# Kernel optimization log

Hardware: AMD Instinct MI355X
Metric: run time of the kernel (lower is better)

## Reference

```python
import jax, jax.numpy as jnp
import numpy as np

N, L, H, V = 8192, 512, 64, 50000
NUM_PARENT = 1024


def setup_inputs() -> dict:
    key = jax.random.key(0)
    ks = jax.random.split(key, 12)
    def mat(k, shape):
        return 0.1 * jax.random.normal(k, shape, dtype=jnp.float32)
    return {
        "x_word": jax.random.normal(ks[0], (N, L), dtype=jnp.float32),
        "x_index": jax.random.randint(ks[1], (N, L), 0, V),
        "tree": jax.random.randint(ks[2], (N, 2), 0, N),
        "num_parent": NUM_PARENT,
        "embedding": mat(ks[3], (V, H)),
        "W_z": mat(ks[4], (H, H)),
        "U_z": mat(ks[5], (H, H)),
        "b_z": jnp.zeros((H,), dtype=jnp.float32),
        "W_r": mat(ks[6], (H, H)),
        "U_r": mat(ks[7], (H, H)),
        "b_r": jnp.zeros((H,), dtype=jnp.float32),
        "W_h": mat(ks[8], (H, H)),
        "U_h": mat(ks[9], (H, H)),
        "b_h": jnp.zeros((H,), dtype=jnp.float32),
    }


def _hard_sigmoid(x):
    # torch double-threshold trick == clip(0.2*x + 0.5, 0, 1)
    return jnp.clip(0.2 * x + 0.5, 0.0, 1.0)


def reference(x_word, x_index, tree, num_parent, embedding,
              W_z, U_z, b_z, W_r, U_r, b_r, W_h, U_h, b_h):
    n_nodes = x_word.shape[0]
    hdim = embedding.shape[1]

    def step(node_h, xs):
        word, idx, info = xs  # word: [L] f32, idx: [L] int, info: [2] int
        parent_h = node_h[info[0]]                 # [H]
        child_xe = embedding[idx].T @ word         # [H] weighted embedding sum
        z = _hard_sigmoid(W_z @ child_xe + U_z @ parent_h + b_z)
        r = _hard_sigmoid(W_r @ child_xe + U_r @ parent_h + b_r)
        c = jnp.tanh(W_h @ child_xe + U_h @ (parent_h * r) + b_h)
        h = z * parent_h + (1.0 - z) * c           # [H]
        return node_h.at[info[1]].set(h), h

    node_h0 = jnp.zeros((n_nodes, hdim), dtype=x_word.dtype)
    # original loops i in range(len(x_word) - 1)
    _, child_hs = jax.lax.scan(step, node_h0,
                               (x_word[:-1], x_index[:-1], tree[:-1]))
    # output = max over child_hs[num_parent-1:]
    return jnp.max(child_hs[num_parent - 1:], axis=0)
```

## Files before the change

kernel.cpp:

```cpp
#include <hip/hip_runtime.h>
#include <math.h>

#define NODES  8192
#define STEPS  8191
#define LW     512
#define H      64
#define VOCAB  50000
#define SWEEPK 13

__global__ void ws_too_small_kernel(float* __restrict__ out) {
    if (threadIdx.x < H) out[threadIdx.x] = -12345.0f;
}

__global__ __launch_bounds__(256)
void cvt_emb(const float* __restrict__ emb, unsigned int* __restrict__ embh) {
    int i = blockIdx.x * 256 + threadIdx.x;
    float2 v = reinterpret_cast<const float2*>(emb)[i];
    unsigned int ux = __float_as_uint(v.x);
    unsigned int uy = __float_as_uint(v.y);
    unsigned int bx = (ux + 0x7fffu + ((ux >> 16) & 1u)) >> 16;
    unsigned int by = (uy + 0x7fffu + ((uy >> 16) & 1u)) >> 16;
    embh[i] = bx | (by << 16);
}

__global__ __launch_bounds__(256)
void zero_kernel(int* __restrict__ p) {
    p[blockIdx.x * blockDim.x + threadIdx.x] = 0;
}

__global__ __launch_bounds__(256)
void hist_writers(const int* __restrict__ tree, int* __restrict__ count) {
    int j = blockIdx.x * blockDim.x + threadIdx.x;
    if (j < STEPS) atomicAdd(&count[tree[2 * j + 1]], 1);
}

__global__ __launch_bounds__(1024)
void prefix_kernel(const int* __restrict__ cnt, int* __restrict__ off) {
    __shared__ int wsum[16];
    int tid  = threadIdx.x;
    int lane = tid & 63;
    int wv   = tid >> 6;
    int base = tid * 8;

    int v[8], run = 0;
    #pragma unroll
    for (int e = 0; e < 8; ++e) { v[e] = run; run += cnt[base + e]; }

    int x = run;
    #pragma unroll
    for (int d = 1; d < 64; d <<= 1) {
        int y = __shfl_up(x, d, 64);
        if (lane >= d) x += y;
    }
    if (lane == 63) wsum[wv] = x;
    __syncthreads();
    if (wv == 0) {
        int s = (lane < 16) ? wsum[lane] : 0;
        #pragma unroll
        for (int d = 1; d < 16; d <<= 1) {
            int y = __shfl_up(s, d, 64);
            if (lane >= d) s += y;
        }
        if (lane < 16) wsum[lane] = s;
    }
    __syncthreads();
    int wbase = (wv > 0) ? wsum[wv - 1] : 0;
    int tbase = wbase + x - run;
    #pragma unroll
    for (int e = 0; e < 8; ++e) off[base + e] = tbase + v[e];
    if (tid == 1023) off[8192] = tbase + run;
}

__global__ __launch_bounds__(256)
void scatter_writers(const int* __restrict__ tree, const int* __restrict__ woff,
                     int* __restrict__ cursor, int* __restrict__ writers) {
    int j = blockIdx.x * blockDim.x + threadIdx.x;
    if (j >= STEPS) return;
    int v = tree[2 * j + 1];
    int pos = atomicAdd(&cursor[v], 1);
    writers[woff[v] + pos] = j;
}

__global__ __launch_bounds__(256)
void pred_bucket(const int* __restrict__ tree, const int* __restrict__ woff,
                 const int* __restrict__ writers, int* __restrict__ pred) {
    int i = blockIdx.x * blockDim.x + threadIdx.x;
    if (i >= STEPS) return;
    int v  = tree[2 * i];
    int t0 = woff[v], t1 = woff[v + 1];
    int best = -1;
    for (int t = t0; t < t1; ++t) {
        int j = writers[t];
        if (j < i && j > best) best = j;
    }
    pred[i] = best;
}

__global__ __launch_bounds__(1024)
void fused_sched(const int* __restrict__ pred, int* __restrict__ lstart_g,
                 int* __restrict__ order_g) {
    __shared__ int   smem_i[NODES];
    __shared__ short dep[NODES];
    __shared__ int   wsum[16];
    int tid = threadIdx.x;

    short* jmp = (short*)smem_i;
    for (int i = tid; i < NODES; i += 1024) {
        int p = (i < STEPS) ? pred[i] : -1;
        jmp[i] = (short)p;
        dep[i] = (p >= 0) ? 1 : 0;
    }
    __syncthreads();

    for (int r = 0; r < 13; ++r) {
        short nd[8], nj[8];
        #pragma unroll
        for (int e = 0; e < 8; ++e) {
            int i = tid + e * 1024;
            int j = jmp[i];
            if (j >= 0) { nd[e] = (short)(dep[i] + dep[j]); nj[e] = jmp[j]; }
            else        { nd[e] = dep[i];                   nj[e] = -1;     }
        }
        __syncthreads();
        #pragma unroll
        for (int e = 0; e < 8; ++e) {
            int i = tid + e * 1024;
            dep[i] = nd[e];
            jmp[i] = nj[e];
        }
        __syncthreads();
    }

    int d8[8];
    #pragma unroll
    for (int e = 0; e < 8; ++e) d8[e] = dep[tid + e * 1024];
    __syncthreads();

    int* lcnt = smem_i;
    for (int i = tid; i < NODES; i += 1024) lcnt[i] = 0;
    __syncthreads();
    #pragma unroll
    for (int e = 0; e < 8; ++e) {
        int i = tid + e * 1024;
        if (i < STEPS) atomicAdd(&lcnt[d8[e]], 1);
    }
    __syncthreads();

    {
        int lane = tid & 63, wv = tid >> 6, base = tid * 8;
        int v[8], run = 0;
        #pragma unroll
        for (int e = 0; e < 8; ++e) { v[e] = run; run += lcnt[base + e]; }
        int x = run;
        #pragma unroll
        for (int d = 1; d < 64; d <<= 1) {
            int y = __shfl_up(x, d, 64);
            if (lane >= d) x += y;
        }
        if (lane == 63) wsum[wv] = x;
        __syncthreads();
        if (wv == 0) {
            int s = (lane < 16) ? wsum[lane] : 0;
            #pragma unroll
            for (int d = 1; d < 16; d <<= 1) {
                int y = __shfl_up(s, d, 64);
                if (lane >= d) s += y;
            }
            if (lane < 16) wsum[lane] = s;
        }
        __syncthreads();
        int wbase = (wv > 0) ? wsum[wv - 1] : 0;
        int tbase = wbase + x - run;
        #pragma unroll
        for (int e = 0; e < 8; ++e) lstart_g[base + e] = tbase + v[e];
        if (tid == 1023) lstart_g[8192] = tbase + run;
    }
    __threadfence_block();
    __syncthreads();

    for (int i = tid; i < NODES; i += 1024) lcnt[i] = 0;
    __syncthreads();
    #pragma unroll
    for (int e = 0; e < 8; ++e) {
        int i = tid + e * 1024;
        if (i < STEPS) {
            int d = d8[e];
            int pos = atomicAdd(&lcnt[d], 1);
            order_g[lstart_g[d] + pos] = i;
        }
    }
}

__global__ __launch_bounds__(256)
void gather_project(const float* __restrict__ xw, const int* __restrict__ xi,
                    const unsigned short* __restrict__ embh,
                    const float* __restrict__ Wz, const float* __restrict__ Wr,
                    const float* __restrict__ Wh,
                    const float* __restrict__ bz, const float* __restrict__ br,
                    const float* __restrict__ bh,
                    const int* __restrict__ pred,
                    float* __restrict__ A, float* __restrict__ child_h) {
    int i    = blockIdx.x;
    int tid  = threadIdx.x;
    int wave = tid >> 6;
    int lane = tid & 63;
    int g8   = lane >> 3;
    int h8   = (lane & 7) * 8;

    __shared__ float part[4][64];
    __shared__ float xe[64];

    const float* xwi = xw + (size_t)i * LW;
    const int*   xii = xi + (size_t)i * LW;

    float acc[8] = {0.f, 0.f, 0.f, 0.f, 0.f, 0.f, 0.f, 0.f};
    #pragma unroll 4
    for (int it = 0; it < 16; ++it) {
        int l   = wave * 128 + it * 8 + g8;
        int idx = xii[l];
        float w = xwi[l];
        uint4 q = *reinterpret_cast<const uint4*>(embh + ((size_t)idx << 6) + h8);
        acc[0] = fmaf(w, __uint_as_float(q.x << 16),          acc[0]);
        acc[1] = fmaf(w, __uint_as_float(q.x & 0xffff0000u),  acc[1]);
        acc[2] = fmaf(w, __uint_as_float(q.y << 16),          acc[2]);
        acc[3] = fmaf(w, __uint_as_float(q.y & 0xffff0000u),  acc[3]);
        acc[4] = fmaf(w, __uint_as_float(q.z << 16),          acc[4]);
        acc[5] = fmaf(w, __uint_as_float(q.z & 0xffff0000u),  acc[5]);
        acc[6] = fmaf(w, __uint_as_float(q.w << 16),          acc[6]);
        acc[7] = fmaf(w, __uint_as_float(q.w & 0xffff0000u),  acc[7]);
    }
    #pragma unroll
    for (int c = 0; c < 8; ++c) {
        acc[c] += __shfl_xor(acc[c], 8,  64);
        acc[c] += __shfl_xor(acc[c], 16, 64);
        acc[c] += __shfl_xor(acc[c], 32, 64);
    }
    if (lane < 8) {
        #pragma unroll
        for (int c = 0; c < 8; ++c) part[wave][lane * 8 + c] = acc[c];
    }
    __syncthreads();
    if (tid < 64) xe[tid] = part[0][tid] + part[1][tid] + part[2][tid] + part[3][tid];
    __syncthreads();

    float s = 0.f;
    if (tid < 192) {
        int o = tid & 63;
        const float* W = (tid < 64) ? Wz : (tid < 128 ? Wr : Wh);
        const float* b = (tid < 64) ? bz : (tid < 128 ? br : bh);
        s = b[o];
        #pragma unroll
        for (int j = 0; j < H; j += 4) {
            float4 w4 = *reinterpret_cast<const float4*>(W + (size_t)o * H + j);
            s = fmaf(w4.x, xe[j],     s);
            s = fmaf(w4.y, xe[j + 1], s);
            s = fmaf(w4.z, xe[j + 2], s);
            s = fmaf(w4.w, xe[j + 3], s);
        }
    }
    bool isroot = (pred[i] < 0);
    if (tid < 64)                part[0][tid]       = s;
    if (tid >= 128 && tid < 192) part[1][tid - 128] = s;
    __syncthreads();
    if (isroot) {
        if (tid < 64) {
            float z = fminf(fmaxf(0.2f * part[0][tid] + 0.5f, 0.f), 1.f);
            float c = tanhf(part[1][tid]);
            child_h[(size_t)i * H + tid] = (1.f - z) * c;
        }
    } else {
        if (tid < 192) A[(size_t)i * 192 + tid] = s;
    }
}

__device__ __forceinline__ void gru_core(
        int i, int lane, const float* __restrict__ A,
        const int* __restrict__ pred,
        const float* uz, const float* ur, const float* uh,
        float* __restrict__ child_h) {
    int p = pred[i];
    float ph = (p >= 0) ? child_h[(size_t)p * H + lane] : 0.f;
    const float* Ai = A + (size_t)i * 192;
    float az = Ai[lane];
    float ar = Ai[64 + lane];
    float ah = Ai[128 + lane];

    #pragma unroll
    for (int j = 0; j < H; ++j) {
        float s = __shfl(ph, j, 64);
        az = fmaf(uz[j], s, az);
        ar = fmaf(ur[j], s, ar);
    }
    float z = fminf(fmaxf(0.2f * az + 0.5f, 0.f), 1.f);
    float r = fminf(fmaxf(0.2f * ar + 0.5f, 0.f), 1.f);
    float phr = ph * r;
    #pragma unroll
    for (int j = 0; j < H; ++j) {
        float s = __shfl(phr, j, 64);
        ah = fmaf(uh[j], s, ah);
    }
    float c = tanhf(ah);
    child_h[(size_t)i * H + lane] = z * ph + (1.f - z) * c;
}

__global__ __launch_bounds__(256)
void sweep_lvl(int k, const int* __restrict__ lstart, const int* __restrict__ order,
               const float* __restrict__ A, const int* __restrict__ pred,
               const float* __restrict__ Uz, const float* __restrict__ Ur,
               const float* __restrict__ Uh, float* __restrict__ child_h) {
    int s0 = lstart[k], s1 = lstart[k + 1];
    int wave = (blockIdx.x * blockDim.x + threadIdx.x) >> 6;
    int lane = threadIdx.x & 63;
    if (s0 + wave >= s1) return;

    float uz[H], ur[H], uh[H];
    #pragma unroll
    for (int j = 0; j < H; j += 4) {
        float4 a4 = *reinterpret_cast<const float4*>(Uz + (size_t)lane * H + j);
        uz[j] = a4.x; uz[j+1] = a4.y; uz[j+2] = a4.z; uz[j+3] = a4.w;
        float4 b4 = *reinterpret_cast<const float4*>(Ur + (size_t)lane * H + j);
        ur[j] = b4.x; ur[j+1] = b4.y; ur[j+2] = b4.z; ur[j+3] = b4.w;
        float4 c4 = *reinterpret_cast<const float4*>(Uh + (size_t)lane * H + j);
        uh[j] = c4.x; uh[j+1] = c4.y; uh[j+2] = c4.z; uh[j+3] = c4.w;
    }
    for (int t = s0 + wave; t < s1; t += 512)
        gru_core(order[t], lane, A, pred, uz, ur, uh, child_h);
}

__global__ __launch_bounds__(1024)
void tail_block(const int* __restrict__ lstart, const int* __restrict__ order,
                const float* __restrict__ A, const int* __restrict__ pred,
                const float* __restrict__ Uz, const float* __restrict__ Ur,
                const float* __restrict__ Uh, float* __restrict__ child_h) {
    int wave = threadIdx.x >> 6;
    int lane = threadIdx.x & 63;
    for (int k = SWEEPK; k < NODES; ++k) {
        int s0 = lstart[k];
        if (s0 >= STEPS) break;
        int s1 = lstart[k + 1];
        for (int t = s0 + wave; t < s1; t += 16) {
            float uz[H], ur[H], uh[H];
            #pragma unroll
            for (int j = 0; j < H; j += 4) {
                float4 a4 = *reinterpret_cast<const float4*>(Uz + (size_t)lane * H + j);
                uz[j] = a4.x; uz[j+1] = a4.y; uz[j+2] = a4.z; uz[j+3] = a4.w;
                float4 b4 = *reinterpret_cast<const float4*>(Ur + (size_t)lane * H + j);
                ur[j] = b4.x; ur[j+1] = b4.y; ur[j+2] = b4.z; ur[j+3] = b4.w;
                float4 c4 = *reinterpret_cast<const float4*>(Uh + (size_t)lane * H + j);
                uh[j] = c4.x; uh[j+1] = c4.y; uh[j+2] = c4.z; uh[j+3] = c4.w;
            }
            gru_core(order[t], lane, A, pred, uz, ur, uh, child_h);
        }
        __syncthreads();
    }
}

__global__ __launch_bounds__(256)
void reduce_partial(const float* __restrict__ child_h,
                    const int* __restrict__ np_ptr,
                    float* __restrict__ partial) {
    int b   = blockIdx.x;
    int tid = threadIdx.x;
    int h   = tid & 63;
    int grp = tid >> 6;
    int np    = *np_ptr;
    int start = np - 1;
    int total = STEPS - start;
    int per   = (total + gridDim.x - 1) / gridDim.x;
    int r0 = start + b * per;
    int r1 = r0 + per; if (r1 > STEPS) r1 = STEPS;
    float m = -INFINITY;
    for (int row = r0 + grp; row < r1; row += 4)
        m = fmaxf(m, child_h[(size_t)row * H + h]);
    __shared__ float sm[4][64];
    sm[grp][h] = m;
    __syncthreads();
    if (tid < 64)
        partial[b * 64 + tid] = fmaxf(fmaxf(sm[0][tid], sm[1][tid]),
                                      fmaxf(sm[2][tid], sm[3][tid]));
}

__global__ void reduce_final(const float* __restrict__ partial,
                             float* __restrict__ out, int nb) {
    int h = threadIdx.x;
    float m = -INFINITY;
    for (int b = 0; b < nb; ++b) m = fmaxf(m, partial[b * 64 + h]);
    out[h] = m;
}

extern "C" void kernel_launch(void* const* d_in, const int* in_sizes, int n_in,
                              void* d_out, int out_size, void* d_ws, size_t ws_size,
                              hipStream_t stream) {
    const float* xw   = (const float*)d_in[0];
    const int*   xi   = (const int*)  d_in[1];
    const int*   tree = (const int*)  d_in[2];
    const int*   np   = (const int*)  d_in[3];
    const float* emb  = (const float*)d_in[4];
    const float* Wz   = (const float*)d_in[5];
    const float* Uz   = (const float*)d_in[6];
    const float* bz   = (const float*)d_in[7];
    const float* Wr   = (const float*)d_in[8];
    const float* Ur   = (const float*)d_in[9];
    const float* br   = (const float*)d_in[10];
    const float* Wh   = (const float*)d_in[11];
    const float* Uh   = (const float*)d_in[12];
    const float* bh   = (const float*)d_in[13];

    size_t bA   = (size_t)STEPS * 192 * 4;
    size_t bCH  = (size_t)STEPS * H   * 4;
    size_t bEH  = (size_t)VOCAB * H   * 2;
    size_t bInt = (size_t)(8192 * 5 + 8256 * 2) * 4;
    size_t bPar = 56 * 64 * 4 + 256;
    size_t need = bA + bCH + bEH + bInt + bPar;
    if (ws_size < need) {
        ws_too_small_kernel<<<1, 64, 0, stream>>>((float*)d_out);
        return;
    }

    char* base = (char*)d_ws;
    float*          A       = (float*)base;                 base += bA;
    float*          child_h = (float*)base;                 base += bCH;
    unsigned short* embh    = (unsigned short*)base;        base += bEH;
    int*            pred    = (int*)base;
    int*            writers = pred    + 8192;
    int*            order   = writers + 8192;
    int*            count   = order   + 8192;
    int*            cursor  = count   + 8192;
    int*            woff    = cursor  + 8192;
    int*            lstart  = woff    + 8256;
    float*          partial = (float*)(lstart + 8256);

    cvt_emb        <<<6250, 256, 0, stream>>>(emb, (unsigned int*)embh);

    zero_kernel    <<<64,  256, 0, stream>>>(count);
    hist_writers   <<<32,  256, 0, stream>>>(tree, count);
    prefix_kernel  <<<1,  1024, 0, stream>>>(count, woff);
    scatter_writers<<<32,  256, 0, stream>>>(tree, woff, cursor, writers);
    pred_bucket    <<<32,  256, 0, stream>>>(tree, woff, writers, pred);

    fused_sched    <<<1,  1024, 0, stream>>>(pred, lstart, order);

    gather_project <<<STEPS, 256, 0, stream>>>(xw, xi, embh, Wz, Wr, Wh,
                                               bz, br, bh, pred, A, child_h);

    for (int k = 1; k < SWEEPK; ++k)
        sweep_lvl  <<<128, 256, 0, stream>>>(k, lstart, order, A, pred,
                                             Uz, Ur, Uh, child_h);
    tail_block     <<<1, 1024, 0, stream>>>(lstart, order, A, pred,
                                            Uz, Ur, Uh, child_h);

    reduce_partial <<<56,  256, 0, stream>>>(child_h, np, partial);
    reduce_final   <<<1,    64, 0, stream>>>(partial, (float*)d_out, 56);
}
```

Before: 322.0 us.

## Replace level-scheduled sweeps with a flag-driven dataflow scan over dependencies

Drops the single-block level computation (pointer jumping, histogram, ordering) and the per-level sweep launches plus the tail block. In their place is one persistent kernel where waves take steps in order from an atomic counter, spin on a per-node ready flag for the predecessor, then compute and publish their hidden state. This removes the scheduling kernel and the many serialized launches, but adds spin-wait cost and relies on in-order ticket progress across all resident waves to avoid deadlock. A bounded spin limit guards against hangs. The gather loop unroll also goes from 4 to 8.

```diff
diff --git a/kernel.cpp b/kernel.cpp
--- a/kernel.cpp
+++ b/kernel.cpp
@@ -6,7 +6,7 @@
 #define LW     512
 #define H      64
 #define VOCAB  50000
-#define SWEEPK 13
+#define SPIN_LIMIT 50000
 
 __global__ void ws_too_small_kernel(float* __restrict__ out) {
     if (threadIdx.x < H) out[threadIdx.x] = -12345.0f;
@@ -96,101 +96,6 @@
     pred[i] = best;
 }
 
-__global__ __launch_bounds__(1024)
-void fused_sched(const int* __restrict__ pred, int* __restrict__ lstart_g,
-                 int* __restrict__ order_g) {
-    __shared__ int   smem_i[NODES];
-    __shared__ short dep[NODES];
-    __shared__ int   wsum[16];
-    int tid = threadIdx.x;
-
-    short* jmp = (short*)smem_i;
-    for (int i = tid; i < NODES; i += 1024) {
-        int p = (i < STEPS) ? pred[i] : -1;
-        jmp[i] = (short)p;
-        dep[i] = (p >= 0) ? 1 : 0;
-    }
-    __syncthreads();
-
-    for (int r = 0; r < 13; ++r) {
-        short nd[8], nj[8];
-        #pragma unroll
-        for (int e = 0; e < 8; ++e) {
-            int i = tid + e * 1024;
-            int j = jmp[i];
-            if (j >= 0) { nd[e] = (short)(dep[i] + dep[j]); nj[e] = jmp[j]; }
-            else        { nd[e] = dep[i];                   nj[e] = -1;     }
-        }
-        __syncthreads();
-        #pragma unroll
-        for (int e = 0; e < 8; ++e) {
-            int i = tid + e * 1024;
-            dep[i] = nd[e];
-            jmp[i] = nj[e];
-        }
-        __syncthreads();
-    }
-
-    int d8[8];
-    #pragma unroll
-    for (int e = 0; e < 8; ++e) d8[e] = dep[tid + e * 1024];
-    __syncthreads();
-
-    int* lcnt = smem_i;
-    for (int i = tid; i < NODES; i += 1024) lcnt[i] = 0;
-    __syncthreads();
-    #pragma unroll
-    for (int e = 0; e < 8; ++e) {
-        int i = tid + e * 1024;
-        if (i < STEPS) atomicAdd(&lcnt[d8[e]], 1);
-    }
-    __syncthreads();
-
-    {
-        int lane = tid & 63, wv = tid >> 6, base = tid * 8;
-        int v[8], run = 0;
-        #pragma unroll
-        for (int e = 0; e < 8; ++e) { v[e] = run; run += lcnt[base + e]; }
-        int x = run;
-        #pragma unroll
-        for (int d = 1; d < 64; d <<= 1) {
-            int y = __shfl_up(x, d, 64);
-            if (lane >= d) x += y;
-        }
-        if (lane == 63) wsum[wv] = x;
-        __syncthreads();
-        if (wv == 0) {
-            int s = (lane < 16) ? wsum[lane] : 0;
-            #pragma unroll
-            for (int d = 1; d < 16; d <<= 1) {
-                int y = __shfl_up(s, d, 64);
-                if (lane >= d) s += y;
-            }
-            if (lane < 16) wsum[lane] = s;
-        }
-        __syncthreads();
-        int wbase = (wv > 0) ? wsum[wv - 1] : 0;
-        int tbase = wbase + x - run;
-        #pragma unroll
-        for (int e = 0; e < 8; ++e) lstart_g[base + e] = tbase + v[e];
-        if (tid == 1023) lstart_g[8192] = tbase + run;
-    }
-    __threadfence_block();
-    __syncthreads();
-
-    for (int i = tid; i < NODES; i += 1024) lcnt[i] = 0;
-    __syncthreads();
-    #pragma unroll
-    for (int e = 0; e < 8; ++e) {
-        int i = tid + e * 1024;
-        if (i < STEPS) {
-            int d = d8[e];
-            int pos = atomicAdd(&lcnt[d], 1);
-            order_g[lstart_g[d] + pos] = i;
-        }
-    }
-}
-
 __global__ __launch_bounds__(256)
 void gather_project(const float* __restrict__ xw, const int* __restrict__ xi,
                     const unsigned short* __restrict__ embh,
@@ -199,7 +104,8 @@
                     const float* __restrict__ bz, const float* __restrict__ br,
                     const float* __restrict__ bh,
                     const int* __restrict__ pred,
-                    float* __restrict__ A, float* __restrict__ child_h) {
+                    float* __restrict__ A, float* __restrict__ child_h,
+                    int* __restrict__ flag) {
     int i    = blockIdx.x;
     int tid  = threadIdx.x;
     int wave = tid >> 6;
@@ -214,7 +120,7 @@
     const int*   xii = xi + (size_t)i * LW;
 
     float acc[8] = {0.f, 0.f, 0.f, 0.f, 0.f, 0.f, 0.f, 0.f};
-    #pragma unroll 4
+    #pragma unroll 8
     for (int it = 0; it < 16; ++it) {
         int l   = wave * 128 + it * 8 + g8;
         int idx = xii[l];
@@ -268,50 +174,19 @@
             float c = tanhf(part[1][tid]);
             child_h[(size_t)i * H + tid] = (1.f - z) * c;
         }
+        if (tid == 64) flag[i] = 1;
     } else {
         if (tid < 192) A[(size_t)i * 192 + tid] = s;
     }
 }
 
-__device__ __forceinline__ void gru_core(
-        int i, int lane, const float* __restrict__ A,
-        const int* __restrict__ pred,
-        const float* uz, const float* ur, const float* uh,
-        float* __restrict__ child_h) {
-    int p = pred[i];
-    float ph = (p >= 0) ? child_h[(size_t)p * H + lane] : 0.f;
-    const float* Ai = A + (size_t)i * 192;
-    float az = Ai[lane];
-    float ar = Ai[64 + lane];
-    float ah = Ai[128 + lane];
-
-    #pragma unroll
-    for (int j = 0; j < H; ++j) {
-        float s = __shfl(ph, j, 64);
-        az = fmaf(uz[j], s, az);
-        ar = fmaf(ur[j], s, ar);
-    }
-    float z = fminf(fmaxf(0.2f * az + 0.5f, 0.f), 1.f);
-    float r = fminf(fmaxf(0.2f * ar + 0.5f, 0.f), 1.f);
-    float phr = ph * r;
-    #pragma unroll
-    for (int j = 0; j < H; ++j) {
-        float s = __shfl(phr, j, 64);
-        ah = fmaf(uh[j], s, ah);
-    }
-    float c = tanhf(ah);
-    child_h[(size_t)i * H + lane] = z * ph + (1.f - z) * c;
-}
-
-__global__ __launch_bounds__(256)
-void sweep_lvl(int k, const int* __restrict__ lstart, const int* __restrict__ order,
-               const float* __restrict__ A, const int* __restrict__ pred,
+__global__ __launch_bounds__(256)
+void flow_scan(const float* __restrict__ A, const int* __restrict__ pred,
                const float* __restrict__ Uz, const float* __restrict__ Ur,
-               const float* __restrict__ Uh, float* __restrict__ child_h) {
-    int s0 = lstart[k], s1 = lstart[k + 1];
-    int wave = (blockIdx.x * blockDim.x + threadIdx.x) >> 6;
+               const float* __restrict__ Uh,
+               int* __restrict__ flag, int* __restrict__ counter,
+               float* __restrict__ child_h) {
     int lane = threadIdx.x & 63;
-    if (s0 + wave >= s1) return;
 
     float uz[H], ur[H], uh[H];
     #pragma unroll
@@ -323,35 +198,55 @@
         float4 c4 = *reinterpret_cast<const float4*>(Uh + (size_t)lane * H + j);
         uh[j] = c4.x; uh[j+1] = c4.y; uh[j+2] = c4.z; uh[j+3] = c4.w;
     }
-    for (int t = s0 + wave; t < s1; t += 512)
-        gru_core(order[t], lane, A, pred, uz, ur, uh, child_h);
-}
-
-__global__ __launch_bounds__(1024)
-void tail_block(const int* __restrict__ lstart, const int* __restrict__ order,
-                const float* __restrict__ A, const int* __restrict__ pred,
-                const float* __restrict__ Uz, const float* __restrict__ Ur,
-                const float* __restrict__ Uh, float* __restrict__ child_h) {
-    int wave = threadIdx.x >> 6;
-    int lane = threadIdx.x & 63;
-    for (int k = SWEEPK; k < NODES; ++k) {
-        int s0 = lstart[k];
-        if (s0 >= STEPS) break;
-        int s1 = lstart[k + 1];
-        for (int t = s0 + wave; t < s1; t += 16) {
-            float uz[H], ur[H], uh[H];
-            #pragma unroll
-            for (int j = 0; j < H; j += 4) {
-                float4 a4 = *reinterpret_cast<const float4*>(Uz + (size_t)lane * H + j);
-                uz[j] = a4.x; uz[j+1] = a4.y; uz[j+2] = a4.z; uz[j+3] = a4.w;
-                float4 b4 = *reinterpret_cast<const float4*>(Ur + (size_t)lane * H + j);
-                ur[j] = b4.x; ur[j+1] = b4.y; ur[j+2] = b4.z; ur[j+3] = b4.w;
-                float4 c4 = *reinterpret_cast<const float4*>(Uh + (size_t)lane * H + j);
-                uh[j] = c4.x; uh[j+1] = c4.y; uh[j+2] = c4.z; uh[j+3] = c4.w;
+
+    while (true) {
+        int t = 0;
+        if (lane == 0) t = atomicAdd(counter, 1);
+        int i = __builtin_amdgcn_readfirstlane(t);
+        if (i >= STEPS) break;
+
+        int p = pred[i];
+        if (p < 0) continue;
+
+        const float* Ai = A + (size_t)i * 192;
+        float az = Ai[lane];
+        float ar = Ai[64 + lane];
+        float ah = Ai[128 + lane];
+
+        int done = 0, spins = 0;
+        while (!done) {
+            int f = 0;
+            if (lane == 0) f = atomicAdd(&flag[p], 0);
+            done = __builtin_amdgcn_readfirstlane(f);
+            if (!done) {
+                __builtin_amdgcn_s_sleep(1);
+                if (++spins > SPIN_LIMIT) break;
             }
-            gru_core(order[t], lane, A, pred, uz, ur, uh, child_h);
-        }
-        __syncthreads();
+        }
+        __threadfence();
+        float ph = child_h[(size_t)p * H + lane];
+
+        #pragma unroll
+        for (int j = 0; j < H; ++j) {
+            float s = __shfl(ph, j, 64);
+            az = fmaf(uz[j], s, az);
+            ar = fmaf(ur[j], s, ar);
+        }
+        float z = fminf(fmaxf(0.2f * az + 0.5f, 0.f), 1.f);
+        float r = fminf(fmaxf(0.2f * ar + 0.5f, 0.f), 1.f);
+        float phr = ph * r;
+        #pragma unroll
+        for (int j = 0; j < H; ++j) {
+            float s = __shfl(phr, j, 64);
+            ah = fmaf(uh[j], s, ah);
+        }
+        float c    = tanhf(ah);
+        float hval = z * ph + (1.f - z) * c;
+
+        __hip_atomic_store(&child_h[(size_t)i * H + lane], hval,
+                           __ATOMIC_RELAXED, __HIP_MEMORY_SCOPE_AGENT);
+        __threadfence();
+        if (lane == 0) atomicExch(&flag[i], 1);
     }
 }
 
@@ -409,9 +304,9 @@
     size_t bA   = (size_t)STEPS * 192 * 4;
     size_t bCH  = (size_t)STEPS * H   * 4;
     size_t bEH  = (size_t)VOCAB * H   * 2;
-    size_t bInt = (size_t)(8192 * 5 + 8256 * 2) * 4;
+    size_t nInt = 8192 * 2 + 8256 + (8192 * 3 + 256);
     size_t bPar = 56 * 64 * 4 + 256;
-    size_t need = bA + bCH + bEH + bInt + bPar;
+    size_t need = bA + bCH + bEH + nInt * 4 + bPar;
     if (ws_size < need) {
         ws_too_small_kernel<<<1, 64, 0, stream>>>((float*)d_out);
         return;
@@ -423,31 +318,29 @@
     unsigned short* embh    = (unsigned short*)base;        base += bEH;
     int*            pred    = (int*)base;
     int*            writers = pred    + 8192;
-    int*            order   = writers + 8192;
-    int*            count   = order   + 8192;
+    int*            woff    = writers + 8192;
+    int*            zblock  = woff    + 8256;
+    int*            count   = zblock;
     int*            cursor  = count   + 8192;
-    int*            woff    = cursor  + 8192;
-    int*            lstart  = woff    + 8256;
-    float*          partial = (float*)(lstart + 8256);
+    int*            flag    = cursor  + 8192;
+    int*            counter = flag    + 8192;
+    float*          partial = (float*)(counter + 256);
 
     cvt_emb        <<<6250, 256, 0, stream>>>(emb, (unsigned int*)embh);
 
-    zero_kernel    <<<64,  256, 0, stream>>>(count);
+    zero_kernel    <<<97,  256, 0, stream>>>(zblock);
+
     hist_writers   <<<32,  256, 0, stream>>>(tree, count);
     prefix_kernel  <<<1,  1024, 0, stream>>>(count, woff);
     scatter_writers<<<32,  256, 0, stream>>>(tree, woff, cursor, writers);
     pred_bucket    <<<32,  256, 0, stream>>>(tree, woff, writers, pred);
 
-    fused_sched    <<<1,  1024, 0, stream>>>(pred, lstart, order);
-
     gather_project <<<STEPS, 256, 0, stream>>>(xw, xi, embh, Wz, Wr, Wh,
-                                               bz, br, bh, pred, A, child_h);
-
-    for (int k = 1; k < SWEEPK; ++k)
-        sweep_lvl  <<<128, 256, 0, stream>>>(k, lstart, order, A, pred,
-                                             Uz, Ur, Uh, child_h);
-    tail_block     <<<1, 1024, 0, stream>>>(lstart, order, A, pred,
-                                            Uz, Ur, Uh, child_h);
+                                               bz, br, bh, pred, A, child_h,
+                                               flag);
+
+    flow_scan      <<<256, 256, 0, stream>>>(A, pred, Uz, Ur, Uh,
+                                             flag, counter, child_h);
 
     reduce_partial <<<56,  256, 0, stream>>>(child_h, np, partial);
     reduce_final   <<<1,    64, 0, stream>>>(partial, (float*)d_out, 56);
```

Measured after the change: 354.0 us. 1.1x slower.
